# Performance work log

Measured on AMD Instinct MI355X. Metric: run time of the kernel, lower is better.

Reference implementation:

```python
import jax, jax.numpy as jnp
import numpy as np

N = 20000      # nodes
E1 = 100000    # topo (2d) edges
E2 = 100000    # distance edges
HID = 128      # hidden_size
N2D = 128      # node_embed_size_2d
E2D = 64       # edge_embed_size_2d
EF = 128       # edge_feat_size
ET = 32        # edge_type_size
NRBF = 64
CUT = 6.0


def rbf_expand(d):
    # Gaussian radial basis with cosine cutoff envelope, d: [E]
    centers = jnp.linspace(0.0, CUT, NRBF)
    width = CUT / NRBF
    env = 0.5 * (jnp.cos(jnp.pi * jnp.clip(d / CUT, 0.0, 1.0)) + 1.0)
    return jnp.exp(-((d[:, None] - centers) ** 2) / (2.0 * width * width)) * env[:, None]


def setup_inputs() -> dict:
    key = jax.random.key(0)
    ks = jax.random.split(key, 20)
    s = 0.02
    return {
        "H": jax.random.normal(ks[0], (N, HID), jnp.float32),
        "V": jax.random.normal(ks[1], (N, HID, 3), jnp.float32),
        "Z": jax.random.normal(ks[2], (N, 3), jnp.float32) * 3.0,
        "layer_i": 0,
        "H_2d": jax.random.normal(ks[3], (N, N2D), jnp.float32),
        "mask_2d": jnp.ones((N,), bool),
        "E2d_idx": jax.random.randint(ks[4], (2, E1), 0, N),
        "E2d_feat": jax.random.normal(ks[5], (E2D, E1), jnp.float32),
        "Z_3d": jax.random.normal(ks[6], (N, 3), jnp.float32) * 3.0,
        "mask_3d": jnp.ones((N,), bool),
        "Edist_idx": jax.random.randint(ks[7], (2, E2), 0, N),
        "Edist_val": jax.random.uniform(ks[8], (E2,), jnp.float32) * CUT,
        "virtual_node_embed": jax.random.normal(ks[9], (1, N2D), jnp.float32),
        "edge_type_embed": jax.random.normal(ks[10], (3, ET), jnp.float32),
        "W_rbf": jax.random.normal(ks[11], (EF, NRBF), jnp.float32) * s,
        "W_e2d": jax.random.normal(ks[12], (EF, E2D), jnp.float32) * s,
        "W_i": jax.random.normal(ks[13], (HID, HID + N2D), jnp.float32) * s,
        "W_phi1": jax.random.normal(ks[14], (HID, HID + EF + ET), jnp.float32) * s,
        "b_phi1": jnp.zeros((HID,), jnp.float32),
        "W_phi2": jax.random.normal(ks[15], (3 * HID, HID), jnp.float32) * s,
        "b_phi2": jnp.zeros((3 * HID,), jnp.float32),
        "W_msg": jax.random.normal(ks[16], (3 * HID, NRBF), jnp.float32) * s,
        "b_msg": jnp.zeros((3 * HID,), jnp.float32),
    }


def reference(H, V, Z, layer_i, H_2d, mask_2d, E2d_idx, E2d_feat, Z_3d, mask_3d,
              Edist_idx, Edist_val, virtual_node_embed, edge_type_embed,
              W_rbf, W_e2d, W_i, W_phi1, b_phi1, W_phi2, b_phi2, W_msg, b_msg):
    n = H.shape[0]
    # mask_3d is all-True in this fixture => n_cond_3d == n (static shapes)
    nodes_real = jnp.concatenate([H, H_2d], axis=-1)                       # [n, h1+h2]
    virt = jnp.broadcast_to(virtual_node_embed, (n, virtual_node_embed.shape[1]))
    nodes_virt = jnp.concatenate([H, virt], axis=-1)                        # [n, h1+h2]
    nodes = jnp.concatenate([nodes_real, nodes_virt], axis=0) @ W_i.T      # [2n, h1]
    v = jnp.concatenate([V, jnp.zeros_like(V)], axis=0)                     # [2n, h1, 3]
    z = jnp.concatenate([Z, Z_3d], axis=0)                                  # [2n, 3]

    row_3d = jnp.arange(n)
    col_3d = jnp.arange(n) + n
    E3d = jnp.stack([jnp.concatenate([row_3d, col_3d]),
                     jnp.concatenate([col_3d, row_3d])], axis=0)            # [2, 2n]
    edges = jnp.concatenate([E2d_idx, E3d, Edist_idx], axis=-1)             # [2, E]
    e1, e3, e2 = E2d_idx.shape[1], E3d.shape[1], Edist_idx.shape[1]
    edge_type = jnp.concatenate([jnp.zeros((e1,), jnp.int32),
                                 jnp.ones((e3,), jnp.int32),
                                 jnp.full((e2,), 2, jnp.int32)])
    et = edge_type_embed[edge_type]                                         # [E, ET]
    attr2d = E2d_feat.T @ W_e2d.T                                           # [e1, EF]
    attr3d = jnp.zeros((e3, W_e2d.shape[0]), jnp.float32)                   # [e3, EF]
    attrd = rbf_expand(Edist_val) @ W_rbf.T                                 # [e2, EF]
    edge_attr = jnp.concatenate(
        [jnp.concatenate([attr2d, attr3d, attrd], axis=0), et], axis=-1)    # [E, EF+ET]

    # AdapterLayer: PaiNN-style equivariant message passing
    row, col = edges[0], edges[1]
    rel = z[row] - z[col]                                                   # [E, 3]
    dist = jnp.sqrt(jnp.sum(rel * rel, axis=-1) + 1e-8)                     # [E]
    unit = rel / dist[:, None]
    phi_in = jnp.concatenate([nodes[col], edge_attr], axis=-1)
    phi = jax.nn.silu(phi_in @ W_phi1.T + b_phi1) @ W_phi2.T + b_phi2       # [E, 3h]
    wd = rbf_expand(dist) @ W_msg.T + b_msg                                 # [E, 3h]
    m = phi * wd
    h = nodes.shape[1]
    s_msg, v_gate, r_gate = m[:, :h], m[:, h:2 * h], m[:, 2 * h:]
    dv = v[col] * v_gate[:, :, None] + unit[:, None, :] * r_gate[:, :, None]  # [E, h, 3]
    nn2 = nodes.shape[0]
    H_add = jax.ops.segment_sum(s_msg, row, num_segments=nn2)[:n]
    V_add = jax.ops.segment_sum(dv, row, num_segments=nn2)[:n]

    # eval-mode clamp
    H_add = jnp.clip(H_add, -100.0, 100.0)
    V_add = jnp.clip(V_add, -100.0, 100.0)

    mask_dist = jnp.zeros((n,), bool).at[Edist_idx[0]].set(True).at[Edist_idx[1]].set(True)
    update_mask = mask_2d | mask_3d | mask_dist
    H_add = jnp.where(update_mask[:, None], H_add, 0.0)
    V_add = jnp.where(update_mask[:, None, None], V_add, 0.0)
    return H_add, V_add
```

## Files before the change

kernel.cpp:

```cpp
#include <hip/hip_runtime.h>
#include <hip/hip_bf16.h>

#define NN   20000
#define E1N  100000
#define E2N  100000
#define NEFF 220000
#define TILE 64
#define NBLK ((NEFF + TILE - 1) / TILE)
#define NPAD (NBLK * TILE)
#define RBF_STEP   0.09523809523809523f
#define RBF_INV2W2 56.88888888888889f

typedef short  bf16x8 __attribute__((ext_vector_type(8)));
typedef float  f32x4  __attribute__((ext_vector_type(4)));

__device__ __forceinline__ float4 ld4(const float* p) {
    return *reinterpret_cast<const float4*>(p);
}
__device__ __forceinline__ ushort f2bf(float x) {
    __hip_bfloat16 h = __float2bfloat16(x);
    return *reinterpret_cast<ushort*>(&h);
}
__device__ __forceinline__ float bf2f(ushort u) {
    return __uint_as_float(((unsigned)u) << 16);
}
__device__ __forceinline__ float env_of(float d) {
    float x = fminf(fmaxf(d * (1.0f / 6.0f), 0.0f), 1.0f);
    return 0.5f * (__cosf(3.14159265358979f * x) + 1.0f);
}

__device__ __forceinline__ int edge_row(int eid, const int* __restrict__ E2d_idx,
                                        const int* __restrict__ Edist_idx) {
    if (eid < E1N) return E2d_idx[eid];
    if (eid < E1N + NN) return eid - E1N;
    return Edist_idx[eid - E1N - NN];
}

__global__ __launch_bounds__(256) void hist_kernel(
    const int* __restrict__ E2d_idx, const int* __restrict__ Edist_idx,
    int* __restrict__ hist) {
    int g = blockIdx.x * 256 + threadIdx.x;
    if (g < NEFF) atomicAdd(&hist[edge_row(g, E2d_idx, Edist_idx)], 1);
}

__global__ __launch_bounds__(1024) void scan_kernel(
    const int* __restrict__ hist, int* __restrict__ start, int* __restrict__ cursor) {
    __shared__ int buf[1024];
    __shared__ int carry;
    const int t = threadIdx.x;
    if (t == 0) carry = 0;
    __syncthreads();
    for (int chunk = 0; chunk < 20; ++chunk) {
        int idx = chunk * 1024 + t;
        int v = (idx < NN) ? hist[idx] : 0;
        buf[t] = v;
        __syncthreads();
        for (int off = 1; off < 1024; off <<= 1) {
            int x = (t >= off) ? buf[t - off] : 0;
            __syncthreads();
            buf[t] += x;
            __syncthreads();
        }
        int excl  = buf[t] - v;
        int cbase = carry;
        int tot   = buf[1023];
        if (idx <= NN) {
            start[idx] = cbase + excl;
            if (idx < NN) cursor[idx] = cbase + excl;
        }
        __syncthreads();
        if (t == 0) carry = cbase + tot;
        __syncthreads();
    }
}

__global__ __launch_bounds__(256) void scatter_kernel(
    const int* __restrict__ E2d_idx, const int* __restrict__ Edist_idx,
    int* __restrict__ cursor, int* __restrict__ order) {
    int g = blockIdx.x * 256 + threadIdx.x;
    if (g < NEFF) {
        int r = edge_row(g, E2d_idx, Edist_idx);
        int pos = atomicAdd(&cursor[r], 1);
        order[pos] = g;
    }
}

__global__ __launch_bounds__(64) void chunkrow_kernel(
    const int* __restrict__ order, const int* __restrict__ E2d_idx,
    const int* __restrict__ Edist_idx, int cap, int nch, int* __restrict__ chunk_r0) {
    int i = threadIdx.x;
    if (i < nch) {
        int p = i * cap;
        if (p >= NEFF) p = NEFF - 1;
        chunk_r0[i] = edge_row(order[p], E2d_idx, Edist_idx);
    }
}

__global__ __launch_bounds__(256) void meta_kernel(
    const int* __restrict__ order, const int* __restrict__ E2d_idx,
    const int* __restrict__ Edist_idx, const float* __restrict__ Edist_val,
    const float* __restrict__ Z, const float* __restrict__ Z3d,
    int4* __restrict__ metaI, float4* __restrict__ metaF,
    float4* __restrict__ payloadU) {
    int g = blockIdx.x * 256 + threadIdx.x;
    if (g >= NPAD) return;
    int eid = (g < NEFF) ? order[g] : -1;
    int row, col, ty, e2 = 0; float dval = 0.f;
    if (eid < 0)             { ty = 1; row = -1; col = 0; }
    else if (eid < E1N)      { ty = 0; row = E2d_idx[eid]; col = E2d_idx[E1N + eid]; e2 = eid; }
    else if (eid < E1N + NN) { ty = 1; int jj = eid - E1N; row = jj; col = jj + NN; }
    else { ty = 2; int g2 = eid - E1N - NN;
           row = Edist_idx[g2]; col = Edist_idx[E2N + g2]; dval = Edist_val[g2]; }
    int rs = (row < 0) ? 0 : row;
    float prx = Z[rs * 3], pry = Z[rs * 3 + 1], prz = Z[rs * 3 + 2];
    float pcx, pcy, pcz;
    if (col < NN) { pcx = Z[col * 3]; pcy = Z[col * 3 + 1]; pcz = Z[col * 3 + 2]; }
    else { int c = col - NN; pcx = Z3d[c * 3]; pcy = Z3d[c * 3 + 1]; pcz = Z3d[c * 3 + 2]; }
    float dx = prx - pcx, dy = pry - pcy, dz = prz - pcz;
    float dist = sqrtf(dx * dx + dy * dy + dz * dz + 1e-8f);
    float inv = 1.0f / dist;
    int vcol = (col < NN) ? col : -1;
    metaI[g] = make_int4(col, row, ty, e2);
    metaF[g] = make_float4(dist, dval, env_of(dist), env_of(dval));
    if (row >= 0)
        payloadU[g] = make_float4(dx * inv, dy * inv, dz * inv, __int_as_float(vcol));
}

__global__ __launch_bounds__(256) void prep_kernel(
    const float* __restrict__ W_phi1, const float* __restrict__ b_phi1,
    const float* __restrict__ W_e2d, const float* __restrict__ W_rbf,
    const float* __restrict__ W_phi2, const float* __restrict__ W_msg,
    const float* __restrict__ et,
    ushort* __restrict__ W1c, ushort* __restrict__ W2b,
    ushort* __restrict__ Wmb, float* __restrict__ b_type) {
    int g = blockIdx.x * 256 + threadIdx.x;
    if (g < 32768) {
        int n = g >> 8, k = g & 255;
        float v;
        if (k < 128) v = W_phi1[n * 288 + k];
        else {
            int kk = k - 128;
            const float* Wsel = (kk < 64) ? W_e2d : W_rbf;
            int j = kk & 63;
            float s = 0.f;
            for (int a = 0; a < 128; ++a) s += W_phi1[n * 288 + 128 + a] * Wsel[a * 64 + j];
            v = s;
        }
        W1c[n * 256 + k] = f2bf(v);
    } else if (g < 32768 + 49152) {
        int q = g - 32768; W2b[q] = f2bf(W_phi2[q]);
    } else if (g < 32768 + 49152 + 24576) {
        int q = g - 81920; Wmb[q] = f2bf(W_msg[q]);
    } else if (g < 32768 + 49152 + 24576 + 384) {
        int q = g - 106496; int ty = q >> 7, n = q & 127;
        float s = b_phi1[n];
        for (int a = 0; a < 32; ++a) s += W_phi1[n * 288 + 256 + a] * et[ty * 32 + a];
        b_type[q] = s;
    }
}

__global__ __launch_bounds__(256) void featT_kernel(
    const float* __restrict__ feat, ushort* __restrict__ featTb) {
    __shared__ float tile[64][65];
    const int t = threadIdx.x;
    const int cbase = blockIdx.x * 64;
    for (int i = t; i < 64 * 64; i += 256) {
        int k = i >> 6, e = i & 63;
        tile[k][e] = (cbase + e < E1N) ? feat[(size_t)k * E1N + cbase + e] : 0.f;
    }
    __syncthreads();
    for (int i = t; i < 64 * 64; i += 256) {
        int e = i >> 6, k = i & 63;
        if (cbase + e < E1N) featTb[(size_t)(cbase + e) * 64 + k] = f2bf(tile[k][e]);
    }
}

__global__ __launch_bounds__(256) void nodes_kernel(
    const float* __restrict__ H, const float* __restrict__ H2d,
    const float* __restrict__ virt, const float* __restrict__ Wi,
    ushort* __restrict__ nodesb) {
    __shared__ float x[16][256];
    const int t = threadIdx.x;
    const int rbase = blockIdx.x * 16;

    for (int i = t; i < 16 * 64; i += 256) {
        int r = i >> 6, q = i & 63;
        int row = rbase + r;
        float4 v;
        if (row < NN) {
            v = (q < 32) ? ld4(H + row * 128 + q * 4) : ld4(H2d + row * 128 + (q - 32) * 4);
        } else {
            int rr = row - NN;
            v = (q < 32) ? ld4(H + rr * 128 + q * 4) : ld4(virt + (q - 32) * 4);
        }
        *reinterpret_cast<float4*>(&x[r][q * 4]) = v;
    }
    __syncthreads();

    const int j = t & 127;
    const int rg = t >> 7;
    float acc[8] = {0.f, 0.f, 0.f, 0.f, 0.f, 0.f, 0.f, 0.f};
    for (int k4 = 0; k4 < 64; ++k4) {
        float4 w = ld4(Wi + j * 256 + k4 * 4);
#pragma unroll
        for (int r = 0; r < 8; ++r) {
            float4 xv = *reinterpret_cast<const float4*>(&x[rg * 8 + r][k4 * 4]);
            acc[r] += w.x * xv.x + w.y * xv.y + w.z * xv.z + w.w * xv.w;
        }
    }
#pragma unroll
    for (int r = 0; r < 8; ++r)
        nodesb[(rbase + rg * 8 + r) * 128 + j] = f2bf(acc[r]);
}

template <int MODE>
__global__ __launch_bounds__(256, 2) void edge_kernel(
    const ushort* __restrict__ nodesb, const float* __restrict__ V,
    const float* __restrict__ Z, const float* __restrict__ Z3d,
    const int* __restrict__ E2d_idx, const float* __restrict__ E2d_feat,
    const ushort* __restrict__ featTb,
    const int* __restrict__ Edist_idx, const float* __restrict__ Edist_val,
    const ushort* __restrict__ W1c, const ushort* __restrict__ W2b,
    const ushort* __restrict__ Wmb, const float* __restrict__ b_type,
    const float* __restrict__ b_phi2, const float* __restrict__ b_msg,
    const int4* __restrict__ metaI, const float4* __restrict__ metaF,
    int p0, ushort* __restrict__ payloadM,
    float* __restrict__ Hout, float* __restrict__ Vout) {

    __shared__ ushort A1[TILE][264];
    __shared__ ushort WB[128][132];
    __shared__ float  s_bt[3][128];
    __shared__ int    s_row[TILE], s_col[TILE], s_ty[TILE], s_e2[TILE], s_vcol[TILE];
    __shared__ float  s_dist[TILE], s_dval[TILE], s_env[TILE], s_env2[TILE];
    __shared__ float  s_unit[TILE][3];

    ushort (*hid)[136] = reinterpret_cast<ushort(*)[136]>(&A1[0][0]);
    ushort* m_lds = &A1[0][0] + 8704;

    const int t = threadIdx.x;
    const int gbase = blockIdx.x * TILE;

    if (MODE == 1) {
        if (t < TILE) {
            int4 mi = metaI[p0 + gbase + t];
            s_col[t] = mi.x; s_row[t] = mi.y; s_ty[t] = mi.z; s_e2[t] = mi.w;
        } else if (t < 2 * TILE) {
            int e = t - TILE;
            float4 mf = metaF[p0 + gbase + e];
            s_dist[e] = mf.x; s_dval[e] = mf.y; s_env[e] = mf.z; s_env2[e] = mf.w;
        }
    } else {
        if (t < TILE) {
            int gpos = gbase + t;
            int eid = (gpos < NEFF) ? gpos : -1;
            int row, col, ty, e2 = 0; float dval = 0.f;
            if (eid < 0)             { ty = 1; row = -1; col = 0; }
            else if (eid < E1N)      { ty = 0; row = E2d_idx[eid]; col = E2d_idx[E1N + eid]; e2 = eid; }
            else if (eid < E1N + NN) { ty = 1; int jj = eid - E1N; row = jj; col = jj + NN; }
            else { ty = 2; int g2 = eid - E1N - NN;
                   row = Edist_idx[g2]; col = Edist_idx[E2N + g2]; dval = Edist_val[g2]; }
            int rs = (row < 0) ? 0 : row;
            float prx = Z[rs * 3], pry = Z[rs * 3 + 1], prz = Z[rs * 3 + 2];
            float pcx, pcy, pcz;
            if (col < NN) { pcx = Z[col * 3]; pcy = Z[col * 3 + 1]; pcz = Z[col * 3 + 2]; }
            else { int c = col - NN; pcx = Z3d[c * 3]; pcy = Z3d[c * 3 + 1]; pcz = Z3d[c * 3 + 2]; }
            float dx = prx - pcx, dy = pry - pcy, dz = prz - pcz;
            float dist = sqrtf(dx * dx + dy * dy + dz * dz + 1e-8f);
            float inv = 1.0f / dist;
            s_row[t] = row; s_col[t] = col; s_ty[t] = ty; s_e2[t] = e2;
            s_vcol[t] = (col < NN) ? col : -1;
            s_unit[t][0] = dx * inv; s_unit[t][1] = dy * inv; s_unit[t][2] = dz * inv;
            s_dist[t] = dist; s_dval[t] = dval;
            s_env[t] = env_of(dist); s_env2[t] = env_of(dval);
        }
    }
    for (int i = t; i < 384; i += 256) ((float*)s_bt)[i] = b_type[i];
    __syncthreads();

    for (int i = t; i < TILE * 16; i += 256) {
        int e = i >> 4, q = i & 15;
        *reinterpret_cast<uint4*>(&A1[e][q * 8]) =
            *reinterpret_cast<const uint4*>(nodesb + (size_t)s_col[e] * 128 + q * 8);
    }
    if (MODE == 1) {
        for (int i = t; i < TILE * 128; i += 256) {
            int e = i >> 7, k = i & 127;
            int ty = s_ty[e];
            ushort v = 0;
            if (ty == 0) { if (k < 64) v = featTb[(size_t)s_e2[e] * 64 + k]; }
            else if (ty == 2) {
                if (k >= 64) {
                    float dd = s_dval[e] - (float)(k - 64) * RBF_STEP;
                    v = f2bf(__expf(-dd * dd * RBF_INV2W2) * s_env2[e]);
                }
            }
            A1[e][128 + k] = v;
        }
    } else {
        for (int i = t; i < TILE * 128; i += 256) {
            int k = i >> 6, e = i & 63;
            int ty = s_ty[e];
            float v = 0.f;
            if (ty == 0) { if (k < 64) v = E2d_feat[(size_t)k * E1N + s_e2[e]]; }
            else if (ty == 2) {
                if (k >= 64) {
                    float dd = s_dval[e] - (float)(k - 64) * RBF_STEP;
                    v = __expf(-dd * dd * RBF_INV2W2) * s_env2[e];
                }
            }
            A1[e][128 + k] = f2bf(v);
        }
    }
    for (int i = t; i < 128 * 16; i += 256) {
        int n = i >> 4, q = i & 15;
        *reinterpret_cast<uint4*>(&WB[n][q * 8]) =
            *reinterpret_cast<const uint4*>(W1c + (size_t)n * 256 + q * 8);
    }
    __syncthreads();

    const int w  = t >> 6, lane = t & 63;
    const int mh = w >> 1, nh = w & 1;
    const int lr = lane >> 4, lc = lane & 15;
    const int ar0 = mh * 32 + lc;

    bf16x8 ra0[2], ra1[2];
    {
        float dA = s_dist[ar0],      eA = s_env[ar0];
        float dB = s_dist[ar0 + 16], eB = s_env[ar0 + 16];
#pragma unroll
        for (int ks = 0; ks < 2; ++ks)
#pragma unroll
            for (int j = 0; j < 8; ++j) {
                float c  = (float)(ks * 32 + lr * 8 + j) * RBF_STEP;
                float tA = dA - c, tB = dB - c;
                ra0[ks][j] = (short)f2bf(__expf(-tA * tA * RBF_INV2W2) * eA);
                ra1[ks][j] = (short)f2bf(__expf(-tB * tB * RBF_INV2W2) * eB);
            }
    }

    f32x4 acc[2][4];
#pragma unroll
    for (int mt = 0; mt < 2; ++mt)
#pragma unroll
        for (int nt = 0; nt < 4; ++nt) acc[mt][nt] = (f32x4){0.f, 0.f, 0.f, 0.f};
#pragma unroll
    for (int ks = 0; ks < 4; ++ks) {
        bf16x8 a0 = *reinterpret_cast<const bf16x8*>(&A1[ar0][ks * 32 + lr * 8]);
        bf16x8 a1 = *reinterpret_cast<const bf16x8*>(&A1[ar0 + 16][ks * 32 + lr * 8]);
#pragma unroll
        for (int nt = 0; nt < 4; ++nt) {
            int n = nh * 64 + nt * 16 + lc;
            bf16x8 b = *reinterpret_cast<const bf16x8*>(&WB[n][ks * 32 + lr * 8]);
            acc[0][nt] = __builtin_amdgcn_mfma_f32_16x16x32_bf16(a0, b, acc[0][nt], 0, 0, 0);
            acc[1][nt] = __builtin_amdgcn_mfma_f32_16x16x32_bf16(a1, b, acc[1][nt], 0, 0, 0);
        }
    }
    __syncthreads();
    for (int i = t; i < 128 * 16; i += 256) {
        int n = i >> 4, q = i & 15;
        *reinterpret_cast<uint4*>(&WB[n][q * 8]) =
            *reinterpret_cast<const uint4*>(W1c + (size_t)n * 256 + 128 + q * 8);
    }
    __syncthreads();
#pragma unroll
    for (int ks = 4; ks < 8; ++ks) {
        bf16x8 a0 = *reinterpret_cast<const bf16x8*>(&A1[ar0][ks * 32 + lr * 8]);
        bf16x8 a1 = *reinterpret_cast<const bf16x8*>(&A1[ar0 + 16][ks * 32 + lr * 8]);
#pragma unroll
        for (int nt = 0; nt < 4; ++nt) {
            int n = nh * 64 + nt * 16 + lc;
            bf16x8 b = *reinterpret_cast<const bf16x8*>(&WB[n][(ks - 4) * 32 + lr * 8]);
            acc[0][nt] = __builtin_amdgcn_mfma_f32_16x16x32_bf16(a0, b, acc[0][nt], 0, 0, 0);
            acc[1][nt] = __builtin_amdgcn_mfma_f32_16x16x32_bf16(a1, b, acc[1][nt], 0, 0, 0);
        }
    }
    __syncthreads();

#pragma unroll
    for (int mt = 0; mt < 2; ++mt)
#pragma unroll
        for (int nt = 0; nt < 4; ++nt)
#pragma unroll
            for (int r = 0; r < 4; ++r) {
                int e  = mh * 32 + mt * 16 + lr * 4 + r;
                int ch = nh * 64 + nt * 16 + lc;
                float x = acc[mt][nt][r] + s_bt[s_ty[e]][ch];
                hid[e][ch] = f2bf(x / (1.0f + __expf(-x)));
            }
    for (int i = t; i < 128 * 16; i += 256) {
        int n = i >> 4, q = i & 15;
        *reinterpret_cast<uint4*>(&WB[n][q * 8]) =
            *reinterpret_cast<const uint4*>(W2b + (size_t)n * 128 + q * 8);
    }
    __syncthreads();

    bf16x8 ha0[4], ha1[4];
#pragma unroll
    for (int ks = 0; ks < 4; ++ks) {
        ha0[ks] = *reinterpret_cast<const bf16x8*>(&hid[ar0][ks * 32 + lr * 8]);
        ha1[ks] = *reinterpret_cast<const bf16x8*>(&hid[ar0 + 16][ks * 32 + lr * 8]);
    }

    f32x4 vgr[2][4];
#pragma unroll
    for (int c = 0; c < 3; ++c) {
        f32x4 p[2][4], g[2][4];
#pragma unroll
        for (int mt = 0; mt < 2; ++mt)
#pragma unroll
            for (int nt = 0; nt < 4; ++nt) {
                p[mt][nt] = (f32x4){0.f, 0.f, 0.f, 0.f};
                g[mt][nt] = (f32x4){0.f, 0.f, 0.f, 0.f};
            }
#pragma unroll
        for (int ks = 0; ks < 4; ++ks) {
#pragma unroll
            for (int nt = 0; nt < 4; ++nt) {
                int n = nh * 64 + nt * 16 + lc;
                bf16x8 b = *reinterpret_cast<const bf16x8*>(&WB[n][ks * 32 + lr * 8]);
                p[0][nt] = __builtin_amdgcn_mfma_f32_16x16x32_bf16(ha0[ks], b, p[0][nt], 0, 0, 0);
                p[1][nt] = __builtin_amdgcn_mfma_f32_16x16x32_bf16(ha1[ks], b, p[1][nt], 0, 0, 0);
            }
        }
#pragma unroll
        for (int ks = 0; ks < 2; ++ks) {
#pragma unroll
            for (int nt = 0; nt < 4; ++nt) {
                int n = c * 128 + nh * 64 + nt * 16 + lc;
                bf16x8 b = *reinterpret_cast<const bf16x8*>(Wmb + (size_t)n * 64 + ks * 32 + lr * 8);
                g[0][nt] = __builtin_amdgcn_mfma_f32_16x16x32_bf16(ra0[ks], b, g[0][nt], 0, 0, 0);
                g[1][nt] = __builtin_amdgcn_mfma_f32_16x16x32_bf16(ra1[ks], b, g[1][nt], 0, 0, 0);
            }
        }
        __syncthreads();
        if (c < 2) {
            for (int i = t; i < 128 * 16; i += 256) {
                int n = i >> 4, q = i & 15;
                *reinterpret_cast<uint4*>(&WB[n][q * 8]) =
                    *reinterpret_cast<const uint4*>(W2b + (size_t)((c + 1) * 128 + n) * 128 + q * 8);
            }
        }
#pragma unroll
        for (int mt = 0; mt < 2; ++mt)
#pragma unroll
            for (int nt = 0; nt < 4; ++nt) {
                int d  = nh * 64 + nt * 16 + lc;
                float b2 = b_phi2[c * 128 + d];
                float bm = b_msg[c * 128 + d];
#pragma unroll
                for (int r = 0; r < 4; ++r) {
                    int e = mh * 32 + mt * 16 + lr * 4 + r;
                    float m = (p[mt][nt][r] + b2) * (g[mt][nt][r] + bm);
                    if (MODE == 1) {
                        m_lds[e * 128 + d] = f2bf(m);
                    } else {
                        int row = s_row[e];
                        if (c == 0) {
                            if (row >= 0) unsafeAtomicAdd(&Hout[(size_t)row * 128 + d], m);
                        } else if (c == 1) {
                            vgr[mt][nt][r] = m;
                        } else if (row >= 0) {
                            float vgv = vgr[mt][nt][r];
                            int vc = s_vcol[e];
                            float vx = 0.f, vy = 0.f, vz = 0.f;
                            if (vc >= 0) {
                                const float* vp = V + ((size_t)vc * 128 + d) * 3;
                                vx = vp[0]; vy = vp[1]; vz = vp[2];
                            }
                            float* vo = Vout + ((size_t)row * 128 + d) * 3;
                            unsafeAtomicAdd(vo + 0, vx * vgv + s_unit[e][0] * m);
                            unsafeAtomicAdd(vo + 1, vy * vgv + s_unit[e][1] * m);
                            unsafeAtomicAdd(vo + 2, vz * vgv + s_unit[e][2] * m);
                        }
                    }
                }
            }
        __syncthreads();
        if (MODE == 1) {
            for (int i = t; i < 1024; i += 256) {
                int e = i >> 4, q = i & 15;
                *reinterpret_cast<uint4*>(payloadM + (size_t)(gbase + e) * 384 + c * 128 + q * 8) =
                    *reinterpret_cast<const uint4*>(m_lds + e * 128 + q * 8);
            }
        }
    }
}

__global__ __launch_bounds__(256) void reduce_kernel(
    const ushort* __restrict__ payloadM, const float4* __restrict__ payloadU,
    const float* __restrict__ V, const int* __restrict__ start,
    const int* __restrict__ chunk_r0, int ci, int p0, int p1,
    float* __restrict__ Hout, float* __restrict__ Vout) {
    const int t = threadIdx.x;
    const int rbase = chunk_r0[ci] + blockIdx.x * 8;
    const bool hside = (t < 128);
    const int d = hside ? t : (t - 128);
    for (int nr = 0; nr < 8; ++nr) {
        int r = rbase + nr;
        if (r >= NN) return;
        int s0 = start[r], s1 = start[r + 1];
        if (s0 >= p1) return;
        int a = (s0 > p0) ? s0 : p0;
        int b = (s1 < p1) ? s1 : p1;
        if (a >= b) continue;
        if (hside) {
            float acc = 0.f;
            for (int i = a; i < b; ++i) acc += bf2f(payloadM[(size_t)(i - p0) * 384 + d]);
            float* ptr = &Hout[(size_t)r * 128 + d];
            float o = *ptr + acc;
            if (s1 <= p1) o = fminf(fmaxf(o, -100.f), 100.f);
            *ptr = o;
        } else {
            float ax = 0.f, ay = 0.f, az = 0.f;
            for (int i = a; i < b; ++i) {
                const ushort* pm = payloadM + (size_t)(i - p0) * 384;
                float vg = bf2f(pm[128 + d]), rg = bf2f(pm[256 + d]);
                float4 u = payloadU[i];
                int vc = __float_as_int(u.w);
                if (vc >= 0) {
                    const float* vp = V + (size_t)vc * 384 + d * 3;
                    ax += vg * vp[0]; ay += vg * vp[1]; az += vg * vp[2];
                }
                ax += rg * u.x; ay += rg * u.y; az += rg * u.z;
            }
            float* vo = Vout + (size_t)r * 384 + d * 3;
            float ox = vo[0] + ax, oy = vo[1] + ay, oz = vo[2] + az;
            if (s1 <= p1) {
                ox = fminf(fmaxf(ox, -100.f), 100.f);
                oy = fminf(fmaxf(oy, -100.f), 100.f);
                oz = fminf(fmaxf(oz, -100.f), 100.f);
            }
            vo[0] = ox; vo[1] = oy; vo[2] = oz;
        }
    }
}

extern "C" void kernel_launch(void* const* d_in, const int* in_sizes, int n_in,
                              void* d_out, int out_size, void* d_ws, size_t ws_size,
                              hipStream_t stream) {
    const float* H         = (const float*)d_in[0];
    const float* V         = (const float*)d_in[1];
    const float* Z         = (const float*)d_in[2];
    const float* H2d       = (const float*)d_in[4];
    const int*   E2d_idx   = (const int*)d_in[6];
    const float* E2d_feat  = (const float*)d_in[7];
    const float* Z3d       = (const float*)d_in[8];
    const int*   Edist_idx = (const int*)d_in[10];
    const float* Edist_val = (const float*)d_in[11];
    const float* virt      = (const float*)d_in[12];
    const float* et        = (const float*)d_in[13];
    const float* W_rbf     = (const float*)d_in[14];
    const float* W_e2d     = (const float*)d_in[15];
    const float* W_i       = (const float*)d_in[16];
    const float* W_phi1    = (const float*)d_in[17];
    const float* b_phi1    = (const float*)d_in[18];
    const float* W_phi2    = (const float*)d_in[19];
    const float* b_phi2    = (const float*)d_in[20];
    const float* W_msg     = (const float*)d_in[21];
    const float* b_msg     = (const float*)d_in[22];

    ushort* nodesb  = (ushort*)d_ws;
    ushort* W1c     = nodesb + 5120000;
    ushort* W2b     = W1c + 32768;
    ushort* Wmb     = W2b + 49152;
    float*  b_type  = (float*)(Wmb + 24576);
    ushort* featTb  = (ushort*)(b_type + 384);
    int*    hist    = (int*)(featTb + (size_t)E1N * 64);
    int*    cursor  = hist + NN;
    int*    start   = cursor + NN;
    int*    order   = start + NN + 1;
    int*    chunk_r0= order + NPAD;
    int4*   metaI   = (int4*)(((size_t)(chunk_r0 + 64) + 15) & ~(size_t)15);
    float4* metaF   = (float4*)(metaI + NPAD);
    float4* payloadU= metaF + NPAD;

    size_t fixed = (size_t)((char*)(payloadU + NPAD) - (char*)d_ws);
    size_t poff  = (fixed + 255) & ~(size_t)255;
    size_t avail = (ws_size > poff) ? (ws_size - poff) : 0;
    long long cap_ll = (long long)(avail / 768) / TILE * TILE;
    int cap = (cap_ll > (long long)NPAD) ? NPAD : (int)cap_ll;
    const bool big = (cap >= 4096);
    ushort* payloadM = (ushort*)((char*)d_ws + poff);

    float* Hout = (float*)d_out;
    float* Vout = Hout + (size_t)NN * 128;

    hipMemsetAsync(d_out, 0, (size_t)out_size * sizeof(float), stream);
    prep_kernel<<<(32768 + 49152 + 24576 + 384 + 255) / 256, 256, 0, stream>>>(
        W_phi1, b_phi1, W_e2d, W_rbf, W_phi2, W_msg, et, W1c, W2b, Wmb, b_type);
    nodes_kernel<<<(2 * NN) / 16, 256, 0, stream>>>(H, H2d, virt, W_i, nodesb);

    if (big) {
        hipMemsetAsync(hist, 0, NN * sizeof(int), stream);
        featT_kernel<<<(E1N + 63) / 64, 256, 0, stream>>>(E2d_feat, featTb);
        hist_kernel<<<(NEFF + 255) / 256, 256, 0, stream>>>(E2d_idx, Edist_idx, hist);
        scan_kernel<<<1, 1024, 0, stream>>>(hist, start, cursor);
        scatter_kernel<<<(NEFF + 255) / 256, 256, 0, stream>>>(E2d_idx, Edist_idx, cursor, order);
        meta_kernel<<<(NPAD + 255) / 256, 256, 0, stream>>>(
            order, E2d_idx, Edist_idx, Edist_val, Z, Z3d, metaI, metaF, payloadU);
        int bpc = cap / TILE;
        int nch = (NBLK + bpc - 1) / bpc;
        chunkrow_kernel<<<1, 64, 0, stream>>>(order, E2d_idx, Edist_idx, cap, nch, chunk_r0);
        int rbound = (NN < cap + 1) ? NN : (cap + 1);
        int rgrid  = (rbound + 7) / 8;
        for (int ci = 0; ci < nch; ++ci) {
            int b0 = ci * bpc;
            int nb = ((NBLK - b0) < bpc) ? (NBLK - b0) : bpc;
            int p0 = b0 * TILE;
            int p1 = p0 + nb * TILE; if (p1 > NEFF) p1 = NEFF;
            edge_kernel<1><<<nb, 256, 0, stream>>>(
                nodesb, V, Z, Z3d, E2d_idx, E2d_feat, featTb, Edist_idx, Edist_val,
                W1c, W2b, Wmb, b_type, b_phi2, b_msg, metaI, metaF, p0, payloadM,
                Hout, Vout);
            reduce_kernel<<<rgrid, 256, 0, stream>>>(payloadM, payloadU, V, start,
                                                     chunk_r0, ci, p0, p1, Hout, Vout);
        }
    } else {
        edge_kernel<0><<<NBLK, 256, 0, stream>>>(
            nodesb, V, Z, Z3d, E2d_idx, E2d_feat, featTb, Edist_idx, Edist_val,
            W1c, W2b, Wmb, b_type, b_phi2, b_msg, metaI, metaF, 0, payloadM,
            Hout, Vout);
    }
}
```

Measured before the change: 481.9 us.

## Use bf16 MFMA for node projection, pad message LDS, unroll segment reductions

Replaces the scalar fp32 node-projection GEMM with a bf16 MFMA kernel that stages inputs and a bf16 copy of W_i (converted in prep_kernel) through LDS. The message staging buffer in the edge kernel is padded from a 128 to a 132 stride to reduce LDS bank conflicts, with the copy-out narrowed to 8-byte chunks. The segmented H and V reductions are unrolled with multiple independent accumulators to expose more memory-level parallelism. Node inputs are now rounded to bf16 before the projection, which lowers precision somewhat.

```diff
diff --git a/kernel.cpp b/kernel.cpp
--- a/kernel.cpp
+++ b/kernel.cpp
@@ -130,9 +130,10 @@
     const float* __restrict__ W_phi1, const float* __restrict__ b_phi1,
     const float* __restrict__ W_e2d, const float* __restrict__ W_rbf,
     const float* __restrict__ W_phi2, const float* __restrict__ W_msg,
-    const float* __restrict__ et,
+    const float* __restrict__ et, const float* __restrict__ W_i,
     ushort* __restrict__ W1c, ushort* __restrict__ W2b,
-    ushort* __restrict__ Wmb, float* __restrict__ b_type) {
+    ushort* __restrict__ Wmb, float* __restrict__ b_type,
+    ushort* __restrict__ Wib) {
     int g = blockIdx.x * 256 + threadIdx.x;
     if (g < 32768) {
         int n = g >> 8, k = g & 255;
@@ -147,15 +148,17 @@
             v = s;
         }
         W1c[n * 256 + k] = f2bf(v);
-    } else if (g < 32768 + 49152) {
+    } else if (g < 81920) {
         int q = g - 32768; W2b[q] = f2bf(W_phi2[q]);
-    } else if (g < 32768 + 49152 + 24576) {
+    } else if (g < 106496) {
         int q = g - 81920; Wmb[q] = f2bf(W_msg[q]);
-    } else if (g < 32768 + 49152 + 24576 + 384) {
+    } else if (g < 106880) {
         int q = g - 106496; int ty = q >> 7, n = q & 127;
         float s = b_phi1[n];
         for (int a = 0; a < 32; ++a) s += W_phi1[n * 288 + 256 + a] * et[ty * 32 + a];
         b_type[q] = s;
+    } else if (g < 139648) {
+        int q = g - 106880; Wib[q] = f2bf(W_i[q]);
     }
 }
 
@@ -175,42 +178,84 @@
     }
 }
 
-__global__ __launch_bounds__(256) void nodes_kernel(
+__global__ __launch_bounds__(256, 2) void nodes_mfma_kernel(
     const float* __restrict__ H, const float* __restrict__ H2d,
-    const float* __restrict__ virt, const float* __restrict__ Wi,
+    const float* __restrict__ virt, const ushort* __restrict__ Wib,
     ushort* __restrict__ nodesb) {
-    __shared__ float x[16][256];
+    __shared__ ushort A[64][264];
+    __shared__ ushort WB[128][132];
+
     const int t = threadIdx.x;
-    const int rbase = blockIdx.x * 16;
-
-    for (int i = t; i < 16 * 64; i += 256) {
-        int r = i >> 6, q = i & 63;
-        int row = rbase + r;
+    const int gbase = blockIdx.x * 64;
+
+    for (int i = t; i < 64 * 64; i += 256) {
+        int e = i >> 6, q = i & 63;
+        int row = gbase + e;
         float4 v;
-        if (row < NN) {
-            v = (q < 32) ? ld4(H + row * 128 + q * 4) : ld4(H2d + row * 128 + (q - 32) * 4);
-        } else {
-            int rr = row - NN;
-            v = (q < 32) ? ld4(H + rr * 128 + q * 4) : ld4(virt + (q - 32) * 4);
-        }
-        *reinterpret_cast<float4*>(&x[r][q * 4]) = v;
-    }
-    __syncthreads();
-
-    const int j = t & 127;
-    const int rg = t >> 7;
-    float acc[8] = {0.f, 0.f, 0.f, 0.f, 0.f, 0.f, 0.f, 0.f};
-    for (int k4 = 0; k4 < 64; ++k4) {
-        float4 w = ld4(Wi + j * 256 + k4 * 4);
-#pragma unroll
-        for (int r = 0; r < 8; ++r) {
-            float4 xv = *reinterpret_cast<const float4*>(&x[rg * 8 + r][k4 * 4]);
-            acc[r] += w.x * xv.x + w.y * xv.y + w.z * xv.z + w.w * xv.w;
-        }
-    }
-#pragma unroll
-    for (int r = 0; r < 8; ++r)
-        nodesb[(rbase + rg * 8 + r) * 128 + j] = f2bf(acc[r]);
+        if (q < 32)          v = ld4(H + (size_t)((row < NN) ? row : row - NN) * 128 + q * 4);
+        else if (row < NN)   v = ld4(H2d + (size_t)row * 128 + (q - 32) * 4);
+        else                 v = ld4(virt + (q - 32) * 4);
+        ushort tmp[4] = {f2bf(v.x), f2bf(v.y), f2bf(v.z), f2bf(v.w)};
+        *reinterpret_cast<uint2*>(&A[e][q * 4]) = *reinterpret_cast<const uint2*>(tmp);
+    }
+    for (int i = t; i < 128 * 16; i += 256) {
+        int n = i >> 4, q = i & 15;
+        *reinterpret_cast<uint4*>(&WB[n][q * 8]) =
+            *reinterpret_cast<const uint4*>(Wib + (size_t)n * 256 + q * 8);
+    }
+    __syncthreads();
+
+    const int w  = t >> 6, lane = t & 63;
+    const int mh = w >> 1, nh = w & 1;
+    const int lr = lane >> 4, lc = lane & 15;
+    const int ar0 = mh * 32 + lc;
+
+    f32x4 acc[2][4];
+#pragma unroll
+    for (int mt = 0; mt < 2; ++mt)
+#pragma unroll
+        for (int nt = 0; nt < 4; ++nt) acc[mt][nt] = (f32x4){0.f, 0.f, 0.f, 0.f};
+#pragma unroll
+    for (int ks = 0; ks < 4; ++ks) {
+        bf16x8 a0 = *reinterpret_cast<const bf16x8*>(&A[ar0][ks * 32 + lr * 8]);
+        bf16x8 a1 = *reinterpret_cast<const bf16x8*>(&A[ar0 + 16][ks * 32 + lr * 8]);
+#pragma unroll
+        for (int nt = 0; nt < 4; ++nt) {
+            int n = nh * 64 + nt * 16 + lc;
+            bf16x8 b = *reinterpret_cast<const bf16x8*>(&WB[n][ks * 32 + lr * 8]);
+            acc[0][nt] = __builtin_amdgcn_mfma_f32_16x16x32_bf16(a0, b, acc[0][nt], 0, 0, 0);
+            acc[1][nt] = __builtin_amdgcn_mfma_f32_16x16x32_bf16(a1, b, acc[1][nt], 0, 0, 0);
+        }
+    }
+    __syncthreads();
+    for (int i = t; i < 128 * 16; i += 256) {
+        int n = i >> 4, q = i & 15;
+        *reinterpret_cast<uint4*>(&WB[n][q * 8]) =
+            *reinterpret_cast<const uint4*>(Wib + (size_t)n * 256 + 128 + q * 8);
+    }
+    __syncthreads();
+#pragma unroll
+    for (int ks = 4; ks < 8; ++ks) {
+        bf16x8 a0 = *reinterpret_cast<const bf16x8*>(&A[ar0][ks * 32 + lr * 8]);
+        bf16x8 a1 = *reinterpret_cast<const bf16x8*>(&A[ar0 + 16][ks * 32 + lr * 8]);
+#pragma unroll
+        for (int nt = 0; nt < 4; ++nt) {
+            int n = nh * 64 + nt * 16 + lc;
+            bf16x8 b = *reinterpret_cast<const bf16x8*>(&WB[n][(ks - 4) * 32 + lr * 8]);
+            acc[0][nt] = __builtin_amdgcn_mfma_f32_16x16x32_bf16(a0, b, acc[0][nt], 0, 0, 0);
+            acc[1][nt] = __builtin_amdgcn_mfma_f32_16x16x32_bf16(a1, b, acc[1][nt], 0, 0, 0);
+        }
+    }
+#pragma unroll
+    for (int mt = 0; mt < 2; ++mt)
+#pragma unroll
+        for (int nt = 0; nt < 4; ++nt)
+#pragma unroll
+            for (int r = 0; r < 4; ++r) {
+                int e  = mh * 32 + mt * 16 + lr * 4 + r;
+                int ch = nh * 64 + nt * 16 + lc;
+                nodesb[(size_t)(gbase + e) * 128 + ch] = f2bf(acc[mt][nt][r]);
+            }
 }
 
 template <int MODE>
@@ -227,15 +272,15 @@
     int p0, ushort* __restrict__ payloadM,
     float* __restrict__ Hout, float* __restrict__ Vout) {
 
-    __shared__ ushort A1[TILE][264];
+    __shared__ ushort A1f[TILE * 264 + 256];
     __shared__ ushort WB[128][132];
     __shared__ float  s_bt[3][128];
     __shared__ int    s_row[TILE], s_col[TILE], s_ty[TILE], s_e2[TILE], s_vcol[TILE];
     __shared__ float  s_dist[TILE], s_dval[TILE], s_env[TILE], s_env2[TILE];
     __shared__ float  s_unit[TILE][3];
 
-    ushort (*hid)[136] = reinterpret_cast<ushort(*)[136]>(&A1[0][0]);
-    ushort* m_lds = &A1[0][0] + 8704;
+    ushort* hidp  = A1f;
+    ushort* m_lds = A1f + 8704;
 
     const int t = threadIdx.x;
     const int gbase = blockIdx.x * TILE;
@@ -279,7 +324,7 @@
 
     for (int i = t; i < TILE * 16; i += 256) {
         int e = i >> 4, q = i & 15;
-        *reinterpret_cast<uint4*>(&A1[e][q * 8]) =
+        *reinterpret_cast<uint4*>(&A1f[e * 264 + q * 8]) =
             *reinterpret_cast<const uint4*>(nodesb + (size_t)s_col[e] * 128 + q * 8);
     }
     if (MODE == 1) {
@@ -294,7 +339,7 @@
                     v = f2bf(__expf(-dd * dd * RBF_INV2W2) * s_env2[e]);
                 }
             }
-            A1[e][128 + k] = v;
+            A1f[e * 264 + 128 + k] = v;
         }
     } else {
         for (int i = t; i < TILE * 128; i += 256) {
@@ -308,7 +353,7 @@
                     v = __expf(-dd * dd * RBF_INV2W2) * s_env2[e];
                 }
             }
-            A1[e][128 + k] = f2bf(v);
+            A1f[e * 264 + 128 + k] = f2bf(v);
         }
     }
     for (int i = t; i < 128 * 16; i += 256) {
@@ -345,8 +390,8 @@
         for (int nt = 0; nt < 4; ++nt) acc[mt][nt] = (f32x4){0.f, 0.f, 0.f, 0.f};
 #pragma unroll
     for (int ks = 0; ks < 4; ++ks) {
-        bf16x8 a0 = *reinterpret_cast<const bf16x8*>(&A1[ar0][ks * 32 + lr * 8]);
-        bf16x8 a1 = *reinterpret_cast<const bf16x8*>(&A1[ar0 + 16][ks * 32 + lr * 8]);
+        bf16x8 a0 = *reinterpret_cast<const bf16x8*>(&A1f[ar0 * 264 + ks * 32 + lr * 8]);
+        bf16x8 a1 = *reinterpret_cast<const bf16x8*>(&A1f[(ar0 + 16) * 264 + ks * 32 + lr * 8]);
 #pragma unroll
         for (int nt = 0; nt < 4; ++nt) {
             int n = nh * 64 + nt * 16 + lc;
@@ -364,8 +409,8 @@
     __syncthreads();
 #pragma unroll
     for (int ks = 4; ks < 8; ++ks) {
-        bf16x8 a0 = *reinterpret_cast<const bf16x8*>(&A1[ar0][ks * 32 + lr * 8]);
-        bf16x8 a1 = *reinterpret_cast<const bf16x8*>(&A1[ar0 + 16][ks * 32 + lr * 8]);
+        bf16x8 a0 = *reinterpret_cast<const bf16x8*>(&A1f[ar0 * 264 + ks * 32 + lr * 8]);
+        bf16x8 a1 = *reinterpret_cast<const bf16x8*>(&A1f[(ar0 + 16) * 264 + ks * 32 + lr * 8]);
 #pragma unroll
         for (int nt = 0; nt < 4; ++nt) {
             int n = nh * 64 + nt * 16 + lc;
@@ -385,7 +430,7 @@
                 int e  = mh * 32 + mt * 16 + lr * 4 + r;
                 int ch = nh * 64 + nt * 16 + lc;
                 float x = acc[mt][nt][r] + s_bt[s_ty[e]][ch];
-                hid[e][ch] = f2bf(x / (1.0f + __expf(-x)));
+                hidp[e * 136 + ch] = f2bf(x / (1.0f + __expf(-x)));
             }
     for (int i = t; i < 128 * 16; i += 256) {
         int n = i >> 4, q = i & 15;
@@ -397,8 +442,8 @@
     bf16x8 ha0[4], ha1[4];
 #pragma unroll
     for (int ks = 0; ks < 4; ++ks) {
-        ha0[ks] = *reinterpret_cast<const bf16x8*>(&hid[ar0][ks * 32 + lr * 8]);
-        ha1[ks] = *reinterpret_cast<const bf16x8*>(&hid[ar0 + 16][ks * 32 + lr * 8]);
+        ha0[ks] = *reinterpret_cast<const bf16x8*>(&hidp[ar0 * 136 + ks * 32 + lr * 8]);
+        ha1[ks] = *reinterpret_cast<const bf16x8*>(&hidp[(ar0 + 16) * 136 + ks * 32 + lr * 8]);
     }
 
     f32x4 vgr[2][4];
@@ -452,7 +497,7 @@
                     int e = mh * 32 + mt * 16 + lr * 4 + r;
                     float m = (p[mt][nt][r] + b2) * (g[mt][nt][r] + bm);
                     if (MODE == 1) {
-                        m_lds[e * 128 + d] = f2bf(m);
+                        m_lds[e * 132 + d] = f2bf(m);
                     } else {
                         int row = s_row[e];
                         if (c == 0) {
@@ -477,10 +522,10 @@
             }
         __syncthreads();
         if (MODE == 1) {
-            for (int i = t; i < 1024; i += 256) {
-                int e = i >> 4, q = i & 15;
-                *reinterpret_cast<uint4*>(payloadM + (size_t)(gbase + e) * 384 + c * 128 + q * 8) =
-                    *reinterpret_cast<const uint4*>(m_lds + e * 128 + q * 8);
+            for (int i = t; i < 2048; i += 256) {
+                int e = i >> 5, q = i & 31;
+                *reinterpret_cast<uint2*>(payloadM + (size_t)(gbase + e) * 384 + c * 128 + q * 4) =
+                    *reinterpret_cast<const uint2*>(m_lds + e * 132 + q * 4);
             }
         }
     }
@@ -503,26 +548,61 @@
         int a = (s0 > p0) ? s0 : p0;
         int b = (s1 < p1) ? s1 : p1;
         if (a >= b) continue;
+        int n = b - a;
         if (hside) {
-            float acc = 0.f;
-            for (int i = a; i < b; ++i) acc += bf2f(payloadM[(size_t)(i - p0) * 384 + d]);
+            const ushort* base = payloadM + (size_t)(a - p0) * 384 + d;
+            float a0 = 0.f, a1 = 0.f, a2 = 0.f, a3 = 0.f;
+            int i = 0;
+            for (; i + 4 <= n; i += 4) {
+                a0 += bf2f(base[(size_t)i * 384]);
+                a1 += bf2f(base[(size_t)(i + 1) * 384]);
+                a2 += bf2f(base[(size_t)(i + 2) * 384]);
+                a3 += bf2f(base[(size_t)(i + 3) * 384]);
+            }
+            for (; i < n; ++i) a0 += bf2f(base[(size_t)i * 384]);
+            float acc = (a0 + a1) + (a2 + a3);
             float* ptr = &Hout[(size_t)r * 128 + d];
             float o = *ptr + acc;
             if (s1 <= p1) o = fminf(fmaxf(o, -100.f), 100.f);
             *ptr = o;
         } else {
+            const ushort* base = payloadM + (size_t)(a - p0) * 384;
+            const float4* ub = payloadU + a;
             float ax = 0.f, ay = 0.f, az = 0.f;
-            for (int i = a; i < b; ++i) {
-                const ushort* pm = payloadM + (size_t)(i - p0) * 384;
-                float vg = bf2f(pm[128 + d]), rg = bf2f(pm[256 + d]);
-                float4 u = payloadU[i];
-                int vc = __float_as_int(u.w);
-                if (vc >= 0) {
-                    const float* vp = V + (size_t)vc * 384 + d * 3;
-                    ax += vg * vp[0]; ay += vg * vp[1]; az += vg * vp[2];
+            float bx = 0.f, by = 0.f, bz = 0.f;
+            int i = 0;
+            for (; i + 2 <= n; i += 2) {
+                const ushort* pm0 = base + (size_t)i * 384;
+                const ushort* pm1 = base + (size_t)(i + 1) * 384;
+                float vg0 = bf2f(pm0[128 + d]), rg0 = bf2f(pm0[256 + d]);
+                float vg1 = bf2f(pm1[128 + d]), rg1 = bf2f(pm1[256 + d]);
+                float4 u0 = ub[i];
+                float4 u1 = ub[i + 1];
+                int vc0 = __float_as_int(u0.w);
+                int vc1 = __float_as_int(u1.w);
+                if (vc0 >= 0) {
+                    const float* vp = V + (size_t)vc0 * 384 + d * 3;
+                    ax += vg0 * vp[0]; ay += vg0 * vp[1]; az += vg0 * vp[2];
                 }
-                ax += rg * u.x; ay += rg * u.y; az += rg * u.z;
-            }
+                if (vc1 >= 0) {
+                    const float* vp = V + (size_t)vc1 * 384 + d * 3;
+                    bx += vg1 * vp[0]; by += vg1 * vp[1]; bz += vg1 * vp[2];
+                }
+                ax += rg0 * u0.x; ay += rg0 * u0.y; az += rg0 * u0.z;
+                bx += rg1 * u1.x; by += rg1 * u1.y; bz += rg1 * u1.z;
+            }
+            if (i < n) {
+                const ushort* pm0 = base + (size_t)i * 384;
+                float vg0 = bf2f(pm0[128 + d]), rg0 = bf2f(pm0[256 + d]);
+                float4 u0 = ub[i];
+                int vc0 = __float_as_int(u0.w);
+                if (vc0 >= 0) {
+                    const float* vp = V + (size_t)vc0 * 384 + d * 3;
+                    ax += vg0 * vp[0]; ay += vg0 * vp[1]; az += vg0 * vp[2];
+                }
+                ax += rg0 * u0.x; ay += rg0 * u0.y; az += rg0 * u0.z;
+            }
+            ax += bx; ay += by; az += bz;
             float* vo = Vout + (size_t)r * 384 + d * 3;
             float ox = vo[0] + ax, oy = vo[1] + ay, oz = vo[2] + az;
             if (s1 <= p1) {
@@ -563,7 +643,8 @@
     ushort* W1c     = nodesb + 5120000;
     ushort* W2b     = W1c + 32768;
     ushort* Wmb     = W2b + 49152;
-    float*  b_type  = (float*)(Wmb + 24576);
+    ushort* Wib     = Wmb + 24576;
+    float*  b_type  = (float*)(Wib + 32768);
     ushort* featTb  = (ushort*)(b_type + 384);
     int*    hist    = (int*)(featTb + (size_t)E1N * 64);
     int*    cursor  = hist + NN;
@@ -586,9 +667,10 @@
     float* Vout = Hout + (size_t)NN * 128;
 
     hipMemsetAsync(d_out, 0, (size_t)out_size * sizeof(float), stream);
-    prep_kernel<<<(32768 + 49152 + 24576 + 384 + 255) / 256, 256, 0, stream>>>(
-        W_phi1, b_phi1, W_e2d, W_rbf, W_phi2, W_msg, et, W1c, W2b, Wmb, b_type);
-    nodes_kernel<<<(2 * NN) / 16, 256, 0, stream>>>(H, H2d, virt, W_i, nodesb);
+    prep_kernel<<<(139648 + 255) / 256, 256, 0, stream>>>(
+        W_phi1, b_phi1, W_e2d, W_rbf, W_phi2, W_msg, et, W_i,
+        W1c, W2b, Wmb, b_type, Wib);
+    nodes_mfma_kernel<<<(2 * NN) / 64, 256, 0, stream>>>(H, H2d, virt, Wib, nodesb);
 
     if (big) {
         hipMemsetAsync(hist, 0, NN * sizeof(int), stream);
```

New measurement: 405.2 us. -15.9%, faster.
